# Optimization experiments

Hardware: AMD Instinct MI355X
Metric: run time of the kernel (lower is better)

## Reference

```python
import jax, jax.numpy as jnp
import numpy as np

B, N, D = 2, 2048, 1024
H, DH = 16, 64
EPS = 1e-5


def _layernorm(t, g, b):
    m = jnp.mean(t, axis=-1, keepdims=True)
    v = jnp.mean(jnp.square(t - m), axis=-1, keepdims=True)
    return (t - m) * jax.lax.rsqrt(v + EPS) * g + b


def setup_inputs() -> dict:
    key = jax.random.key(0)
    ks = jax.random.split(key, 4)
    return {
        "x": jax.random.normal(ks[0], (B, N, D), dtype=jnp.float32),
        "ln_g": jnp.ones((D,), jnp.float32),
        "ln_b": jnp.zeros((D,), jnp.float32),
        "lnc_g": jnp.ones((D,), jnp.float32),
        "lnc_b": jnp.zeros((D,), jnp.float32),
        "Wq": jax.random.normal(ks[1], (D, H * DH), jnp.float32) * 0.02,
        "Wkv": jax.random.normal(ks[2], (D, 2 * H * DH), jnp.float32) * 0.02,
        "Wo": jax.random.normal(ks[3], (H * DH, D), jnp.float32) * 0.02,
    }


def reference(x, ln_g, ln_b, lnc_g, lnc_b, Wq, Wkv, Wo):
    scale = DH ** (-0.5)
    xn = _layernorm(x, ln_g, ln_b)          # self-attn: context = x
    cn = _layernorm(x, lnc_g, lnc_b)
    q = xn @ Wq                              # [b, n, h*d]
    kv = cn @ Wkv
    k, v = jnp.split(kv, 2, axis=-1)
    # b n (h d) -> b h n d
    q = q.reshape(B, N, H, DH).transpose(0, 2, 1, 3)
    k = k.reshape(B, N, H, DH).transpose(0, 2, 1, 3)
    v = v.reshape(B, N, H, DH).transpose(0, 2, 1, 3)
    sim = jnp.einsum("bhnd,bhmd->bhnm", q, k) * scale
    neg = -jnp.finfo(sim.dtype).max
    causal = jnp.tril(jnp.ones((N, N), dtype=bool))  # allow j <= i
    sim = jnp.where(causal[None, None], sim, neg)
    attn = jax.nn.softmax(sim.astype(jnp.float32), axis=-1)
    out = jnp.einsum("bhnm,bhmd->bhnd", attn, v)
    out = out.transpose(0, 2, 1, 3).reshape(B, N, H * DH)
    return out @ Wo
```

## Files before the change

kernel.cpp:

```cpp
#include <hip/hip_runtime.h>
#include <hip/hip_bf16.h>

#define B_  2
#define N_  2048
#define D_  1024
#define H_  16
#define DH_ 64
#define BN_ROWS (B_ * N_)
#define EPS_ 1e-5f
#define QKV_N 3072

typedef __attribute__((ext_vector_type(8))) short bf16x8_t;
typedef __attribute__((ext_vector_type(4))) short bf16x4_t;
typedef __attribute__((ext_vector_type(4))) float f32x4_t;

#define MFMA16(a, b, c) __builtin_amdgcn_mfma_f32_16x16x16bf16_1k(a, b, c, 0, 0, 0)

typedef const unsigned int __attribute__((address_space(1)))* gas_ptr;
typedef unsigned int __attribute__((address_space(3)))* las_ptr;

__device__ __forceinline__ void async16(const unsigned short* g, unsigned short* l) {
    __builtin_amdgcn_global_load_lds((gas_ptr)g, (las_ptr)l, 16, 0, 0);
}

__device__ __forceinline__ unsigned short f2bf(float f) {
    unsigned int u = __float_as_uint(f);
    unsigned int r = u + 0x7FFFu + ((u >> 16) & 1u);
    return (unsigned short)(r >> 16);
}

__device__ __forceinline__ unsigned int pk2bf(float a, float b) {
    __hip_bfloat162 t = __float22bfloat162_rn(float2{a, b});
    return *(unsigned int*)&t;
}

__global__ __launch_bounds__(256) void ln_wt_kernel(
    const float* __restrict__ x,
    const float* __restrict__ g1, const float* __restrict__ b1,
    const float* __restrict__ g2, const float* __restrict__ b2,
    const float* __restrict__ Wq, const float* __restrict__ Wkv,
    const float* __restrict__ Wo,
    unsigned short* __restrict__ xn, unsigned short* __restrict__ cn,
    unsigned short* __restrict__ wqkvT, unsigned short* __restrict__ woT) {
    const int bid = blockIdx.x;
    const int tid = threadIdx.x;

    if (bid < BN_ROWS) {
        const int row = bid;
        const float4 v = ((const float4*)(x + (size_t)row * D_))[tid];

        float s  = v.x + v.y + v.z + v.w;
        float s2 = v.x * v.x + v.y * v.y + v.z * v.z + v.w * v.w;
        #pragma unroll
        for (int off = 32; off > 0; off >>= 1) {
            s  += __shfl_down(s,  off);
            s2 += __shfl_down(s2, off);
        }
        __shared__ float red[8];
        if ((tid & 63) == 0) { red[tid >> 6] = s; red[4 + (tid >> 6)] = s2; }
        __syncthreads();
        const float S  = red[0] + red[1] + red[2] + red[3];
        const float S2 = red[4] + red[5] + red[6] + red[7];
        const float mean = S * (1.0f / D_);
        const float var  = S2 * (1.0f / D_) - mean * mean;
        const float rstd = rsqrtf(var + EPS_);

        const float4 G1 = ((const float4*)g1)[tid];
        const float4 B1 = ((const float4*)b1)[tid];
        const float4 G2 = ((const float4*)g2)[tid];
        const float4 B2 = ((const float4*)b2)[tid];

        float nx[4] = { (v.x - mean) * rstd, (v.y - mean) * rstd,
                        (v.z - mean) * rstd, (v.w - mean) * rstd };
        ushort4 o1, o2;
        o1.x = f2bf(nx[0] * G1.x + B1.x); o1.y = f2bf(nx[1] * G1.y + B1.y);
        o1.z = f2bf(nx[2] * G1.z + B1.z); o1.w = f2bf(nx[3] * G1.w + B1.w);
        o2.x = f2bf(nx[0] * G2.x + B2.x); o2.y = f2bf(nx[1] * G2.y + B2.y);
        o2.z = f2bf(nx[2] * G2.z + B2.z); o2.w = f2bf(nx[3] * G2.w + B2.w);
        ((ushort4*)(xn + (size_t)row * D_))[tid] = o1;
        ((ushort4*)(cn + (size_t)row * D_))[tid] = o2;
    } else {
        const int zz = bid - BN_ROWS;
        const float* src;
        unsigned short* dst;
        int N, t;
        if (zz < 1024)      { src = Wq;  dst = wqkvT;                       N = 1024; t = zz; }
        else if (zz < 3072) { src = Wkv; dst = wqkvT + (size_t)1024 * 1024; N = 2048; t = zz - 1024; }
        else                { src = Wo;  dst = woT;                         N = 1024; t = zz - 3072; }
        const int nb = N / 32;
        const int n0 = (t % nb) * 32, k0 = (t / nb) * 32;

        __shared__ float tile[32][33];
        const int tx = tid & 31, ty = tid >> 5;
        #pragma unroll
        for (int i = 0; i < 4; i++)
            tile[ty + i * 8][tx] = src[(size_t)(k0 + ty + i * 8) * N + n0 + tx];
        __syncthreads();
        #pragma unroll
        for (int i = 0; i < 4; i++)
            dst[(size_t)(n0 + ty + i * 8) * 1024 + k0 + tx] = f2bf(tile[tx][ty + i * 8]);
    }
}

template <int BM, bool FUSED, bool BF16OUT>
__global__ __launch_bounds__(256, 2) void gemm_kernel(
    const unsigned short* __restrict__ A0, const unsigned short* __restrict__ A1,
    const unsigned short* __restrict__ Bt, void* __restrict__ Cv,
    unsigned short* __restrict__ vt, int M, int N, int K) {
    constexpr int WM = BM / 2, MT = WM / 16, AI = BM / 32;
    __shared__ unsigned short As[BM * 64];
    __shared__ unsigned short Bs[128 * 64];
    const int tid = threadIdx.x, lane = tid & 63, w = tid >> 6;
    const int quad = lane >> 4, l16 = lane & 15;
    const int lr8 = lane >> 3, pg8 = lane & 7;
    const int wr = (w >> 1) * WM, wc = (w & 1) * 64;
    const int bm = blockIdx.y * BM, bn = blockIdx.x * 128;
    const unsigned short* A = (FUSED && bn >= 1024) ? A1 : A0;
    const float cscale = (FUSED && bn < 1024) ? 0.180336880111120f : 1.0f;

    f32x4_t acc[MT][4] = {};
    for (int k0 = 0; k0 < K; k0 += 64) {
        #pragma unroll
        for (int i = 0; i < AI; i++) {
            const int rb = w * (BM / 4) + i * 8;
            const int r  = rb + lr8;
            const int g  = pg8 ^ (r & 7);
            async16(&A[(size_t)(bm + r) * K + k0 + g * 8], &As[rb * 64]);
        }
        #pragma unroll
        for (int i = 0; i < 4; i++) {
            const int rb = w * 32 + i * 8;
            const int r  = rb + lr8;
            const int g  = pg8 ^ (r & 7);
            async16(&Bt[(size_t)(bn + r) * K + k0 + g * 8], &Bs[rb * 64]);
        }
        __syncthreads();
        #pragma unroll
        for (int kk = 0; kk < 64; kk += 32) {
            bf16x8_t af[MT], bfr[4];
            const int g0 = (kk >> 3) + quad;
            #pragma unroll
            for (int t = 0; t < MT; t++)
                af[t] = *(const bf16x8_t*)&As[(wr + t * 16 + l16) * 64 +
                                              ((g0 ^ (l16 & 7)) * 8)];
            #pragma unroll
            for (int t = 0; t < 4; t++)
                bfr[t] = *(const bf16x8_t*)&Bs[(wc + t * 16 + l16) * 64 +
                                               ((g0 ^ (l16 & 7)) * 8)];
            #pragma unroll
            for (int mt = 0; mt < MT; mt++)
                #pragma unroll
                for (int nt = 0; nt < 4; nt++)
                    acc[mt][nt] = __builtin_amdgcn_mfma_f32_16x16x32_bf16(
                        af[mt], bfr[nt], acc[mt][nt], 0, 0, 0);
        }
        __syncthreads();
    }

    if (FUSED && bn >= 2048) {
        const int seq0 = bm + wr;
        const int bq = seq0 >> 11;
        const int kt = (seq0 & (N_ - 1)) >> 6;
        #pragma unroll
        for (int nt = 0; nt < 4; nt++) {
            const int c = (bn - 2048) + wc + nt * 16 + l16;
            unsigned short* dst =
                vt + (((size_t)(bq * 32 + kt) * 1024) + c) * 64;
            #pragma unroll
            for (int mt = 0; mt < 4; mt++) {
                uint2 v2 = { pk2bf(acc[mt][nt][0], acc[mt][nt][1]),
                             pk2bf(acc[mt][nt][2], acc[mt][nt][3]) };
                *(uint2*)&dst[mt * 16 + quad * 4] = v2;
            }
        }
        return;
    }

    #pragma unroll
    for (int mt = 0; mt < MT; mt++)
        #pragma unroll
        for (int nt = 0; nt < 4; nt++)
            #pragma unroll
            for (int r = 0; r < 4; r++) {
                const int row = bm + wr + mt * 16 + quad * 4 + r;
                const int col = bn + wc + nt * 16 + l16;
                if (BF16OUT)
                    ((unsigned short*)Cv)[(size_t)row * N + col] =
                        f2bf(acc[mt][nt][r] * cscale);
                else
                    ((float*)Cv)[(size_t)row * N + col] = acc[mt][nt][r];
            }
}

__global__ __launch_bounds__(256, 2) void flash_attn_kernel(
    const unsigned short* __restrict__ qkv, const unsigned short* __restrict__ vt,
    unsigned short* __restrict__ out) {
    __shared__ unsigned short Qs[64 * 64];
    __shared__ unsigned short Ks[2][64 * 64];
    __shared__ unsigned short Vts[2][64 * 64];

    const int tid = threadIdx.x, lane = tid & 63, w = tid >> 6;
    const int quad = lane >> 4, l16 = lane & 15;
    const int lr8 = lane >> 3, pg8 = lane & 7;
    const int bid = blockIdx.x;
    const int bh   = (bid & 7) * 4 + ((bid >> 3) & 3);
    const int pair = bid >> 5;
    const int b = bh >> 4, h = bh & 15;

    const unsigned short* qb  = qkv + (size_t)(b * N_) * QKV_N + h * DH_;
    const unsigned short* kb  = qb + 1024;
    const unsigned short* vtb = vt + ((size_t)(b * 32) * 1024 + h * 64) * 64;

    bf16x4_t ones4;
    #pragma unroll
    for (int j = 0; j < 4; j++) ones4[j] = (short)0x3F80;

    for (int phase = 0; phase < 2; phase++) {
        const int qt = phase ? (31 - pair) : pair;
        const int qs = qt * 64;
        const int niter = qt + 1;

        __syncthreads();

        #pragma unroll
        for (int i = 0; i < 2; i++) {
            const int rb = w * 16 + i * 8;
            const int r  = rb + lr8;
            const int g  = pg8 ^ (r & 7);
            async16(&qb[(size_t)(qs + r) * QKV_N + g * 8], &Qs[rb * 64]);
            async16(&kb[(size_t)r * QKV_N + g * 8], &Ks[0][rb * 64]);
            async16(&vtb[(size_t)r * 64 + g * 8],   &Vts[0][rb * 64]);
        }

        f32x4_t o[4] = {};
        f32x4_t lacc = {};
        bf16x8_t qf[2];

        for (int jt = 0; jt < niter; jt++) {
            __syncthreads();

            if (jt + 1 < niter) {
                const int js = (jt + 1) * 64;
                const int bsel = (jt + 1) & 1;
                #pragma unroll
                for (int i = 0; i < 2; i++) {
                    const int rb = w * 16 + i * 8;
                    const int r  = rb + lr8;
                    const int g  = pg8 ^ (r & 7);
                    async16(&kb[(size_t)(js + r) * QKV_N + g * 8], &Ks[bsel][rb * 64]);
                    async16(&vtb[((size_t)(jt + 1) * 1024 + r) * 64 + g * 8],
                            &Vts[bsel][rb * 64]);
                }
            }
            const int buf = jt & 1;
            const int js = jt * 64;

            if (jt == 0) {
                #pragma unroll
                for (int k2 = 0; k2 < 2; k2++) {
                    const int g0 = k2 * 4 + quad;
                    qf[k2] = *(const bf16x8_t*)&Qs[
                        (w * 16 + l16) * 64 + (g0 ^ (l16 & 7)) * 8];
                }
            }

            f32x4_t s[4] = {};
            #pragma unroll
            for (int k2 = 0; k2 < 2; k2++) {
                const int g0 = k2 * 4 + quad;
                #pragma unroll
                for (int kt = 0; kt < 4; kt++) {
                    const bf16x8_t a = *(const bf16x8_t*)&Ks[buf][
                        (kt * 16 + l16) * 64 + (g0 ^ (l16 & 7)) * 8];
                    s[kt] = __builtin_amdgcn_mfma_f32_16x16x32_bf16(
                        a, qf[k2], s[kt], 0, 0, 0);
                }
            }

            const bool edge = (jt == niter - 1);
            bf16x4_t pf[4];
            #pragma unroll
            for (int kt = 0; kt < 4; kt++) {
                float p[4];
                #pragma unroll
                for (int r = 0; r < 4; r++) {
                    float sv = s[kt][r];
                    if (edge) {
                        const int key = js + kt * 16 + quad * 4 + r;
                        const int qy  = qs + w * 16 + l16;
                        if (key > qy) sv = -3e38f;
                    }
                    p[r] = exp2f(sv);
                }
                uint2 pk = { pk2bf(p[0], p[1]), pk2bf(p[2], p[3]) };
                pf[kt] = *(bf16x4_t*)&pk;
            }

            #pragma unroll
            for (int kt = 0; kt < 4; kt++) {
                const int g = kt * 2 + (quad >> 1);
                const int col = ((g ^ (l16 & 7)) * 8) + (quad & 1) * 4;
                #pragma unroll
                for (int nt = 0; nt < 4; nt++) {
                    const bf16x4_t bv = *(const bf16x4_t*)&Vts[buf][
                        (nt * 16 + l16) * 64 + col];
                    o[nt] = MFMA16(pf[kt], bv, o[nt]);
                }
                lacc = MFMA16(pf[kt], ones4, lacc);
            }
        }

        #pragma unroll
        for (int r = 0; r < 4; r++) {
            const float inv = 1.0f / lacc[r];
            const int query = qs + w * 16 + quad * 4 + r;
            const int row = b * N_ + query;
            #pragma unroll
            for (int nt = 0; nt < 4; nt++) {
                const int col = h * DH_ + nt * 16 + l16;
                out[(size_t)row * (H_ * DH_) + col] = f2bf(o[nt][r] * inv);
            }
        }
    }
}

extern "C" void kernel_launch(void* const* d_in, const int* in_sizes, int n_in,
                              void* d_out, int out_size, void* d_ws, size_t ws_size,
                              hipStream_t stream) {
    const float* x     = (const float*)d_in[0];
    const float* ln_g  = (const float*)d_in[1];
    const float* ln_b  = (const float*)d_in[2];
    const float* lnc_g = (const float*)d_in[3];
    const float* lnc_b = (const float*)d_in[4];
    const float* Wq    = (const float*)d_in[5];
    const float* Wkv   = (const float*)d_in[6];
    const float* Wo    = (const float*)d_in[7];

    char* ws = (char*)d_ws;
    const size_t MB = 1024 * 1024;
    unsigned short* qkv   = (unsigned short*)(ws + 0 * MB);
    unsigned short* vtbuf = (unsigned short*)(ws + 24 * MB);
    unsigned short* xn    = (unsigned short*)(ws + 32 * MB);
    unsigned short* cn    = (unsigned short*)(ws + 40 * MB);
    unsigned short* wqkvT = (unsigned short*)(ws + 48 * MB);
    unsigned short* woT   = (unsigned short*)(ws + 54 * MB);
    unsigned short* ao    = xn;

    ln_wt_kernel<<<8192, 256, 0, stream>>>(
        x, ln_g, ln_b, lnc_g, lnc_b, Wq, Wkv, Wo, xn, cn, wqkvT, woT);

    gemm_kernel<128, true, true>
        <<<dim3(QKV_N / 128, BN_ROWS / 128), 256, 0, stream>>>(
        xn, cn, wqkvT, qkv, vtbuf, BN_ROWS, QKV_N, D_);

    flash_attn_kernel<<<B_ * H_ * 16, 256, 0, stream>>>(qkv, vtbuf, ao);

    gemm_kernel<64, false, false>
        <<<dim3(D_ / 128, BN_ROWS / 64), 256, 0, stream>>>(
        ao, nullptr, woT, (float*)d_out, nullptr, BN_ROWS, D_, H_ * DH_);
}
```

Measured before the change: 185.9 us.

## Software-pipeline flash attention: overlap QK of next tile with PV of previous

Result: faster. 182.2 us (-2.0%).

```diff
diff --git a/kernel.cpp b/kernel.cpp
--- a/kernel.cpp
+++ b/kernel.cpp
@@ -197,7 +197,7 @@
     unsigned short* __restrict__ out) {
     __shared__ unsigned short Qs[64 * 64];
     __shared__ unsigned short Ks[2][64 * 64];
-    __shared__ unsigned short Vts[2][64 * 64];
+    __shared__ unsigned short Vts[3][64 * 64];
 
     const int tid = threadIdx.x, lane = tid & 63, w = tid >> 6;
     const int quad = lane >> 4, l16 = lane & 15;
@@ -222,63 +222,38 @@
 
         __syncthreads();
 
-        #pragma unroll
-        for (int i = 0; i < 2; i++) {
-            const int rb = w * 16 + i * 8;
-            const int r  = rb + lr8;
-            const int g  = pg8 ^ (r & 7);
-            async16(&qb[(size_t)(qs + r) * QKV_N + g * 8], &Qs[rb * 64]);
-            async16(&kb[(size_t)r * QKV_N + g * 8], &Ks[0][rb * 64]);
-            async16(&vtb[(size_t)r * 64 + g * 8],   &Vts[0][rb * 64]);
-        }
-
         f32x4_t o[4] = {};
         f32x4_t lacc = {};
         bf16x8_t qf[2];
-
-        for (int jt = 0; jt < niter; jt++) {
-            __syncthreads();
-
-            if (jt + 1 < niter) {
-                const int js = (jt + 1) * 64;
-                const int bsel = (jt + 1) & 1;
-                #pragma unroll
-                for (int i = 0; i < 2; i++) {
-                    const int rb = w * 16 + i * 8;
-                    const int r  = rb + lr8;
-                    const int g  = pg8 ^ (r & 7);
-                    async16(&kb[(size_t)(js + r) * QKV_N + g * 8], &Ks[bsel][rb * 64]);
-                    async16(&vtb[((size_t)(jt + 1) * 1024 + r) * 64 + g * 8],
-                            &Vts[bsel][rb * 64]);
-                }
-            }
-            const int buf = jt & 1;
-            const int js = jt * 64;
-
-            if (jt == 0) {
-                #pragma unroll
-                for (int k2 = 0; k2 < 2; k2++) {
-                    const int g0 = k2 * 4 + quad;
-                    qf[k2] = *(const bf16x8_t*)&Qs[
-                        (w * 16 + l16) * 64 + (g0 ^ (l16 & 7)) * 8];
-                }
-            }
-
-            f32x4_t s[4] = {};
+        bf16x4_t pf[4];
+
+        auto prefetch = [&](int t) {
+            const int ksel = t & 1, vsel = t % 3;
+            #pragma unroll
+            for (int i = 0; i < 2; i++) {
+                const int rb = w * 16 + i * 8;
+                const int r  = rb + lr8;
+                const int g  = pg8 ^ (r & 7);
+                async16(&kb[(size_t)(t * 64 + r) * QKV_N + g * 8],
+                        &Ks[ksel][rb * 64]);
+                async16(&vtb[((size_t)t * 1024 + r) * 64 + g * 8],
+                        &Vts[vsel][rb * 64]);
+            }
+        };
+        auto do_qk = [&](int kbuf, f32x4_t* s) {
             #pragma unroll
             for (int k2 = 0; k2 < 2; k2++) {
                 const int g0 = k2 * 4 + quad;
                 #pragma unroll
                 for (int kt = 0; kt < 4; kt++) {
-                    const bf16x8_t a = *(const bf16x8_t*)&Ks[buf][
+                    const bf16x8_t a = *(const bf16x8_t*)&Ks[kbuf][
                         (kt * 16 + l16) * 64 + (g0 ^ (l16 & 7)) * 8];
                     s[kt] = __builtin_amdgcn_mfma_f32_16x16x32_bf16(
                         a, qf[k2], s[kt], 0, 0, 0);
                 }
             }
-
-            const bool edge = (jt == niter - 1);
-            bf16x4_t pf[4];
+        };
+        auto do_exp = [&](const f32x4_t* s, int js, bool edge) {
             #pragma unroll
             for (int kt = 0; kt < 4; kt++) {
                 float p[4];
@@ -290,25 +265,59 @@
                         const int qy  = qs + w * 16 + l16;
                         if (key > qy) sv = -3e38f;
                     }
-                    p[r] = exp2f(sv);
+                    p[r] = __builtin_amdgcn_exp2f(sv);
                 }
                 uint2 pk = { pk2bf(p[0], p[1]), pk2bf(p[2], p[3]) };
                 pf[kt] = *(bf16x4_t*)&pk;
             }
-
+        };
+        auto do_pv = [&](int vbuf) {
             #pragma unroll
             for (int kt = 0; kt < 4; kt++) {
                 const int g = kt * 2 + (quad >> 1);
                 const int col = ((g ^ (l16 & 7)) * 8) + (quad & 1) * 4;
                 #pragma unroll
                 for (int nt = 0; nt < 4; nt++) {
-                    const bf16x4_t bv = *(const bf16x4_t*)&Vts[buf][
+                    const bf16x4_t bv = *(const bf16x4_t*)&Vts[vbuf][
                         (nt * 16 + l16) * 64 + col];
                     o[nt] = MFMA16(pf[kt], bv, o[nt]);
                 }
                 lacc = MFMA16(pf[kt], ones4, lacc);
             }
-        }
+        };
+
+        #pragma unroll
+        for (int i = 0; i < 2; i++) {
+            const int rb = w * 16 + i * 8;
+            const int r  = rb + lr8;
+            const int g  = pg8 ^ (r & 7);
+            async16(&qb[(size_t)(qs + r) * QKV_N + g * 8], &Qs[rb * 64]);
+        }
+        prefetch(0);
+        __syncthreads();
+
+        if (niter > 1) prefetch(1);
+        #pragma unroll
+        for (int k2 = 0; k2 < 2; k2++) {
+            const int g0 = k2 * 4 + quad;
+            qf[k2] = *(const bf16x8_t*)&Qs[
+                (w * 16 + l16) * 64 + (g0 ^ (l16 & 7)) * 8];
+        }
+        {
+            f32x4_t s[4] = {};
+            do_qk(0, s);
+            do_exp(s, 0, niter == 1);
+        }
+
+        for (int jt = 1; jt < niter; jt++) {
+            __syncthreads();
+            if (jt + 1 < niter) prefetch(jt + 1);
+            f32x4_t s[4] = {};
+            do_qk(jt & 1, s);
+            do_pv((jt - 1) % 3);
+            do_exp(s, jt * 64, jt == niter - 1);
+        }
+        do_pv((niter - 1) % 3);
 
         #pragma unroll
         for (int r = 0; r < 4; r++) {
```
